# Optimization experiments

Measured on AMD Instinct MI355X. Metric: run time of the kernel, lower is better.

Reference implementation:

```python
import jax, jax.numpy as jnp
import numpy as np
from jax import lax

DIM = 64
NUM_HEADS = 1
HEAD_DIM = DIM // NUM_HEADS
SR = 8  # reduction_ratio
SCALE = HEAD_DIM ** -0.5


def setup_inputs() -> dict:
    key = jax.random.key(0)
    ks = jax.random.split(key, 12)
    s = 0.02
    return {
        "x": jax.random.normal(ks[0], (8, 16384, DIM), dtype=jnp.float32),
        # conv sr: (out_ch, in_ch, kH, kW) torch OIHW layout
        "sr_w": jax.random.normal(ks[1], (DIM, DIM, SR, SR), dtype=jnp.float32) * s,
        "sr_b": jnp.zeros((DIM,), jnp.float32),
        "ln_g": jnp.ones((DIM,), jnp.float32),
        "ln_b": jnp.zeros((DIM,), jnp.float32),
        # torch Linear weights: (out_features, in_features)
        "q_w": jax.random.normal(ks[2], (DIM, DIM), dtype=jnp.float32) * s,
        "q_b": jnp.zeros((DIM,), jnp.float32),
        "kv_w": jax.random.normal(ks[3], (2 * DIM, DIM), dtype=jnp.float32) * s,
        "kv_b": jnp.zeros((2 * DIM,), jnp.float32),
        "proj_w": jax.random.normal(ks[4], (DIM, DIM), dtype=jnp.float32) * s,
        "proj_b": jnp.zeros((DIM,), jnp.float32),
    }


def _layernorm(x, g, b, eps=1e-5):
    mu = jnp.mean(x, axis=-1, keepdims=True)
    var = jnp.var(x, axis=-1, keepdims=True)
    return (x - mu) * lax.rsqrt(var + eps) * g + b


def reference(x, sr_w, sr_b, ln_g, ln_b, q_w, q_b, kv_w, kv_b, proj_w, proj_b):
    B, N, C = x.shape
    H = W = int(N ** 0.5)
    # q: (B, heads, N, head_dim)
    q = (x @ q_w.T + q_b).reshape(B, N, NUM_HEADS, HEAD_DIM).transpose(0, 2, 1, 3)
    # spatial reduction of KV via strided conv + LayerNorm
    x_ = x.transpose(0, 2, 1).reshape(B, C, H, W)
    x_ = lax.conv_general_dilated(
        x_, sr_w, window_strides=(SR, SR), padding="VALID",
        dimension_numbers=("NCHW", "OIHW", "NCHW"))
    x_ = x_ + sr_b[None, :, None, None]
    x_ = x_.reshape(B, C, -1).transpose(0, 2, 1)  # (B, Nr, C)
    x_ = _layernorm(x_, ln_g, ln_b)
    Nr = x_.shape[1]
    kv = (x_ @ kv_w.T + kv_b).reshape(B, Nr, 2, NUM_HEADS, HEAD_DIM)
    kv = kv.transpose(2, 0, 3, 1, 4)  # (2, B, heads, Nr, hd)
    k, v = kv[0], kv[1]
    attn = jnp.einsum("bhnd,bhmd->bhnm", q, k) * SCALE
    attn = jax.nn.softmax(attn, axis=-1)
    out = jnp.einsum("bhnm,bhmd->bhnd", attn, v)
    out = out.transpose(0, 2, 1, 3).reshape(B, N, C)
    return out @ proj_w.T + proj_b
```

## Files before the change

kernel.cpp:

```cpp
#include <hip/hip_runtime.h>
#include <hip/hip_bf16.h>


typedef __attribute__((ext_vector_type(8))) short bf16x8;
typedef __attribute__((ext_vector_type(4))) float f32x4;

__device__ __forceinline__ unsigned short f2bf(float f) {
    union { __hip_bfloat16 h; unsigned short u; } cv;
    cv.h = __hip_bfloat16(f);
    return cv.u;
}
union U8 { uint4 u; bf16x8 v; };
__device__ __forceinline__ bf16x8 pack8(float e0,float e1,float e2,float e3,
                                        float e4,float e5,float e6,float e7){
    U8 r;
    r.u.x = (unsigned)f2bf(e0) | ((unsigned)f2bf(e1)<<16);
    r.u.y = (unsigned)f2bf(e2) | ((unsigned)f2bf(e3)<<16);
    r.u.z = (unsigned)f2bf(e4) | ((unsigned)f2bf(e5)<<16);
    r.u.w = (unsigned)f2bf(e6) | ((unsigned)f2bf(e7)<<16);
    return r.v;
}
__device__ __forceinline__ bf16x8 ldg8(const unsigned short* p){
    U8 r; r.u = *(const uint4*)p; return r.v;
}

__global__ __launch_bounds__(256) void prep_kernel(
    const float* __restrict__ sr_w,
    const float* __restrict__ q_w, const float* __restrict__ q_b,
    const float* __restrict__ proj_w,
    unsigned short* __restrict__ wbp,
    unsigned short* __restrict__ qwb, unsigned short* __restrict__ pwp,
    float* __restrict__ qb_s)
{
    int tid = blockIdx.x * 256 + threadIdx.x;
    {
        int i = tid & 7, n = (tid>>3)&15, g = (tid>>7)&3, ks = (tid>>9)&31,
            kc = (tid>>14)&3, w = tid>>16;
        int co = 16*w + n;
        int k  = kc*1024 + ks*32 + 8*g + i;
        int kh = k >> 9, kw = (k>>6)&7, cin = k & 63;
        wbp[tid] = f2bf(sr_w[co*4096 + cin*64 + kh*8 + kw]);
    }
    if (tid < 4096)   qwb[tid] = f2bf(q_w[tid] * 0.125f);
    if (tid < 4096) {
        int i = tid & 7, g = (tid>>3)&3, s3 = (tid>>5)&1, co = tid>>6;
        int ch = 32*s3 + 16*(i>>2) + 4*g + (i&3);
        pwp[tid] = f2bf(proj_w[co*64 + ch]);
    }
    if (tid < 64) qb_s[tid] = q_b[tid] * 0.125f;
}

__global__ __launch_bounds__(512) void convln_kernel(
    const float* __restrict__ x, const unsigned short* __restrict__ wbp,
    const float* __restrict__ sr_b,
    const float* __restrict__ ln_g, const float* __restrict__ ln_b,
    const float* __restrict__ kv_w, const float* __restrict__ kv_b,
    unsigned short* __restrict__ kbuf, unsigned short* __restrict__ vp)
{
    __shared__ uint4 xsm4[4096];
    char* xsm = (char*)xsm4;
    float* red = (float*)xsm;
    float* ysp = (float*)(xsm + 49152);

    int bid = blockIdx.x;
    int b = bid >> 4, oh = bid & 15;
    int t = threadIdx.x;
    int w = t >> 6, lane = t & 63, g = lane >> 4, n = lane & 15;

    f32x4 acc[4] = {{0,0,0,0},{0,0,0,0},{0,0,0,0},{0,0,0,0}};
    int khl = w >> 1;
    int kwh = w & 1;

    #pragma unroll
    for (int p = 0; p < 2; ++p) {
        const float* slab = x + (size_t)(b*128 + oh*8 + 4*p) * 128 * 64;
        #pragma unroll
        for (int c2 = 0; c2 < 8; ++c2) {
            int eo = (c2*512 + t) * 8;
            float4 v0 = *(const float4*)(slab + eo);
            float4 v1 = *(const float4*)(slab + eo + 4);
            int byte = eo * 2;
            int dst = byte ^ (((byte >> 10) & 7) << 4);
            U8 tmp; tmp.v = pack8(v0.x,v0.y,v0.z,v0.w,v1.x,v1.y,v1.z,v1.w);
            *(uint4*)(xsm + dst) = tmp.u;
        }
        __syncthreads();

        int khp = 4*p + khl;
        int kc  = khp >> 1;
        int swz = (n & 7) << 4;
        #pragma unroll
        for (int j = 0; j < 8; ++j) {
            int ks  = (khp & 1)*16 + kwh*8 + j;
            int kw  = kwh*4 + (j >> 1);
            int cb  = ((j & 1) << 5) + 8*g;
            int byte = khl*16384 + (n*8 + kw)*128 + cb*2;
            U8 Bx; Bx.u = *(const uint4*)(xsm + (byte ^ swz));
            #pragma unroll
            for (int tc = 0; tc < 4; ++tc) {
                bf16x8 A = ldg8(wbp + ((((tc*4 + kc)*32 + ks)*4 + g)*16 + n)*8);
                acc[tc] = __builtin_amdgcn_mfma_f32_16x16x32_bf16(A, Bx.v, acc[tc], 0, 0, 0);
            }
        }
        __syncthreads();
    }

    #pragma unroll
    for (int tc = 0; tc < 4; ++tc) {
        int byte = w*4096 + n*256 + (16*tc + 4*g)*4;
        *(f32x4*)(xsm + (byte ^ ((n & 7) << 4))) = acc[tc];
    }
    __syncthreads();

    int c = lane;
    #pragma unroll
    for (int pp = 0; pp < 2; ++pp) {
        int pos = w + 8*pp;
        int swzp = (pos & 7) << 4;
        float val = sr_b[c];
        #pragma unroll
        for (int w8 = 0; w8 < 8; ++w8)
            val += *(const float*)(xsm + ((w8*4096 + pos*256 + 4*c) ^ swzp));
        float s = val, s2 = val*val;
        #pragma unroll
        for (int o = 32; o >= 1; o >>= 1) {
            s  += __shfl_xor(s,  o, 64);
            s2 += __shfl_xor(s2, o, 64);
        }
        float mean = s * (1.f/64.f);
        float var  = s2 * (1.f/64.f) - mean*mean;
        float y = (val - mean) * rsqrtf(var + 1e-5f) * ln_g[c] + ln_b[c];
        ysp[pos*64 + c] = y;
        int m = oh*16 + pos;
        #pragma unroll
        for (int h = 0; h < 2; ++h) {
            int oc = c + h*64;
            float a2 = kv_b[oc];
            const float* wr = kv_w + oc*64;
            #pragma unroll
            for (int jj = 0; jj < 64; jj += 4) {
                float4 w4 = *(const float4*)(wr + jj);
                a2 += ysp[pos*64+jj]*w4.x + ysp[pos*64+jj+1]*w4.y
                    + ysp[pos*64+jj+2]*w4.z + ysp[pos*64+jj+3]*w4.w;
            }
            if (h == 0) {
                kbuf[(b*256 + m)*64 + c] = f2bf(a2);
            } else {
                int ks2 = m >> 5, hi = (m >> 4) & 1, g2 = (m >> 2) & 3, r = m & 3;
                vp[(size_t)b*16384 + ((ks2*4 + g2)*64 + c)*8 + r + 4*hi] = f2bf(a2);
            }
        }
    }
}

__global__ __launch_bounds__(512) void attn_kernel(
    const float* __restrict__ x,
    const unsigned short* __restrict__ qwb, const float* __restrict__ qb_s,
    const unsigned short* __restrict__ kbuf, const unsigned short* __restrict__ vp,
    const unsigned short* __restrict__ pwp, const float* __restrict__ proj_b,
    float* __restrict__ out)
{
    __shared__ char Ks[32768];
    int bid = blockIdx.x;
    int b = bid >> 7, rt = bid & 127;
    int t = threadIdx.x;
    {
        const char* kb = (const char*)(kbuf + (size_t)b*16384);
        #pragma unroll
        for (int c = 0; c < 4; ++c) {
            int off = (c*512 + t) * 16;
            int dst = off ^ (((off >> 7) & 7) << 4);
            *(uint4*)(Ks + dst) = *(const uint4*)(kb + off);
        }
    }
    __syncthreads();

    int w = t >> 6, lane = t & 63, g = lane >> 4, n = lane & 15;
    int qrow = rt*128 + w*16 + n;
    const float* xr = x + ((size_t)b*16384 + qrow) * 64;
    const char* vpb = (const char*)(vp + (size_t)b*16384);

    f32x4 qacc[4];
    #pragma unroll
    for (int tau = 0; tau < 4; ++tau)
        qacc[tau] = *(const f32x4*)(qb_s + 16*tau + 4*g);
    bf16x8 xq[2];
    #pragma unroll
    for (int s = 0; s < 2; ++s) {
        float4 v0 = *(const float4*)(xr + 32*s + 8*g);
        float4 v1 = *(const float4*)(xr + 32*s + 8*g + 4);
        xq[s] = pack8(v0.x,v0.y,v0.z,v0.w,v1.x,v1.y,v1.z,v1.w);
    }
    #pragma unroll
    for (int tau = 0; tau < 4; ++tau)
        #pragma unroll
        for (int s = 0; s < 2; ++s) {
            bf16x8 A = ldg8(qwb + (16*tau + n)*64 + 32*s + 8*g);
            qacc[tau] = __builtin_amdgcn_mfma_f32_16x16x32_bf16(A, xq[s], qacc[tau], 0,0,0);
        }
    bf16x8 qkB[2];
    #pragma unroll
    for (int s2 = 0; s2 < 2; ++s2)
        qkB[s2] = pack8(qacc[2*s2][0],  qacc[2*s2][1],  qacc[2*s2][2],  qacc[2*s2][3],
                        qacc[2*s2+1][0],qacc[2*s2+1][1],qacc[2*s2+1][2],qacc[2*s2+1][3]);

    float S[16][4];
    #pragma unroll
    for (int tt = 0; tt < 16; ++tt) {
        f32x4 sa = {0.f, 0.f, 0.f, 0.f};
        int m = 16*tt + n;
        int base = m * 128;
        int swz = (m & 7) << 4;
        #pragma unroll
        for (int s2 = 0; s2 < 2; ++s2) {
            int c1 = (32*s2 + 4*g) * 2;
            uint2 d0 = *(const uint2*)(Ks + ((base + c1)      ^ swz));
            uint2 d1 = *(const uint2*)(Ks + ((base + c1 + 32) ^ swz));
            U8 A; A.u = make_uint4(d0.x, d0.y, d1.x, d1.y);
            sa = __builtin_amdgcn_mfma_f32_16x16x32_bf16(A.v, qkB[s2], sa, 0,0,0);
        }
        S[tt][0]=sa[0]; S[tt][1]=sa[1]; S[tt][2]=sa[2]; S[tt][3]=sa[3];
    }

    float rm[16];
    #pragma unroll
    for (int tt = 0; tt < 16; ++tt)
        rm[tt] = fmaxf(fmaxf(S[tt][0],S[tt][1]), fmaxf(S[tt][2],S[tt][3]));
    float m8[8];
    #pragma unroll
    for (int j = 0; j < 8; ++j) m8[j] = fmaxf(rm[2*j], rm[2*j+1]);
    float mx = fmaxf(fmaxf(fmaxf(m8[0],m8[1]),fmaxf(m8[2],m8[3])),
                     fmaxf(fmaxf(m8[4],m8[5]),fmaxf(m8[6],m8[7])));
    mx = fmaxf(mx, __shfl_xor(mx, 16, 64));
    mx = fmaxf(mx, __shfl_xor(mx, 32, 64));
    #pragma unroll
    for (int tt = 0; tt < 16; ++tt)
        #pragma unroll
        for (int r = 0; r < 4; ++r)
            S[tt][r] = __expf(S[tt][r] - mx);
    float rs[16];
    #pragma unroll
    for (int tt = 0; tt < 16; ++tt) rs[tt] = (S[tt][0]+S[tt][1]) + (S[tt][2]+S[tt][3]);
    float s8[8];
    #pragma unroll
    for (int j = 0; j < 8; ++j) s8[j] = rs[2*j] + rs[2*j+1];
    float ssum = ((s8[0]+s8[1])+(s8[2]+s8[3])) + ((s8[4]+s8[5])+(s8[6]+s8[7]));
    ssum += __shfl_xor(ssum, 16, 64);
    ssum += __shfl_xor(ssum, 32, 64);
    float inv = 1.f / ssum;

    f32x4 oacc[4] = {{0,0,0,0},{0,0,0,0},{0,0,0,0},{0,0,0,0}};
    #pragma unroll
    for (int ks = 0; ks < 8; ++ks) {
        bf16x8 Bp = pack8(S[2*ks][0],  S[2*ks][1],  S[2*ks][2],  S[2*ks][3],
                          S[2*ks+1][0],S[2*ks+1][1],S[2*ks+1][2],S[2*ks+1][3]);
        #pragma unroll
        for (int tc = 0; tc < 4; ++tc) {
            U8 A; A.u = *(const uint4*)(vpb + ((ks*4 + g)*64 + 16*tc + n) * 16);
            oacc[tc] = __builtin_amdgcn_mfma_f32_16x16x32_bf16(A.v, Bp, oacc[tc], 0,0,0);
        }
    }

    bf16x8 Bo[2];
    #pragma unroll
    for (int s3 = 0; s3 < 2; ++s3)
        Bo[s3] = pack8(oacc[2*s3][0]*inv,   oacc[2*s3][1]*inv,
                       oacc[2*s3][2]*inv,   oacc[2*s3][3]*inv,
                       oacc[2*s3+1][0]*inv, oacc[2*s3+1][1]*inv,
                       oacc[2*s3+1][2]*inv, oacc[2*s3+1][3]*inv);
    f32x4 pacc[4];
    #pragma unroll
    for (int tf = 0; tf < 4; ++tf)
        pacc[tf] = *(const f32x4*)(proj_b + 16*tf + 4*g);
    #pragma unroll
    for (int tf = 0; tf < 4; ++tf)
        #pragma unroll
        for (int s3 = 0; s3 < 2; ++s3) {
            bf16x8 Aw = ldg8(pwp + (((16*tf + n)*2 + s3)*4 + g)*8);
            pacc[tf] = __builtin_amdgcn_mfma_f32_16x16x32_bf16(Aw, Bo[s3], pacc[tf], 0,0,0);
        }
    float* orow = out + ((size_t)b*16384 + qrow) * 64;
    #pragma unroll
    for (int tf = 0; tf < 4; ++tf)
        *(float4*)(orow + 16*tf + 4*g) = *(float4*)&pacc[tf];
}

extern "C" void kernel_launch(void* const* d_in, const int* in_sizes, int n_in,
                              void* d_out, int out_size, void* d_ws, size_t ws_size,
                              hipStream_t stream)
{
    const float* x      = (const float*)d_in[0];
    const float* sr_w   = (const float*)d_in[1];
    const float* sr_b   = (const float*)d_in[2];
    const float* ln_g   = (const float*)d_in[3];
    const float* ln_b   = (const float*)d_in[4];
    const float* q_w    = (const float*)d_in[5];
    const float* q_b    = (const float*)d_in[6];
    const float* kv_w   = (const float*)d_in[7];
    const float* kv_b   = (const float*)d_in[8];
    const float* proj_w = (const float*)d_in[9];
    const float* proj_b = (const float*)d_in[10];
    float* out = (float*)d_out;

    char* wsb = (char*)d_ws;
    unsigned short* wbp  = (unsigned short*)(wsb);
    unsigned short* kbuf = (unsigned short*)(wsb + 524288);
    unsigned short* vp   = (unsigned short*)(wsb + 786432);
    unsigned short* qwb  = (unsigned short*)(wsb + 1048576);
    unsigned short* pwp  = (unsigned short*)(wsb + 1056768);
    float*          qb_s = (float*)(wsb + 1064960);

    hipLaunchKernelGGL(prep_kernel, dim3(1024), dim3(256), 0, stream,
                       sr_w, q_w, q_b, proj_w, wbp, qwb, pwp, qb_s);
    hipLaunchKernelGGL(convln_kernel, dim3(128), dim3(512), 0, stream,
                       x, wbp, sr_b, ln_g, ln_b, kv_w, kv_b, kbuf, vp);
    hipLaunchKernelGGL(attn_kernel, dim3(1024), dim3(512), 0, stream,
                       x, qwb, qb_s, kbuf, vp, pwp, proj_b, out);
}
```

Measured before the change: 175.2 us.

## Split strided conv across four blocks per output row and coalesce weight prep

The conv+LayerNorm kernel now uses 512 blocks, each handling a quarter of an output row (4 output positions), instead of 128 blocks covering a full row. Each wave now owns one kernel row kh, and the weight layout is reordered to match. The prep kernel stages one output channel's weights in shared memory so it can read them coalesced and write packed 8-element bf16 vectors. The aim is better occupancy across the GPU's CUs and cheaper weight repacking. In exchange, many MFMA lanes are wasted since only 4 of 16 columns are useful, and each block re-reads the full weight tensor from global memory.

```diff
diff --git a/kernel.cpp b/kernel.cpp
--- a/kernel.cpp
+++ b/kernel.cpp
@@ -32,20 +32,34 @@
     unsigned short* __restrict__ qwb, unsigned short* __restrict__ pwp,
     float* __restrict__ qb_s)
 {
-    int tid = blockIdx.x * 256 + threadIdx.x;
-    {
-        int i = tid & 7, n = (tid>>3)&15, g = (tid>>7)&3, ks = (tid>>9)&31,
-            kc = (tid>>14)&3, w = tid>>16;
-        int co = 16*w + n;
-        int k  = kc*1024 + ks*32 + 8*g + i;
-        int kh = k >> 9, kw = (k>>6)&7, cin = k & 63;
-        wbp[tid] = f2bf(sr_w[co*4096 + cin*64 + kh*8 + kw]);
-    }
-    if (tid < 4096)   qwb[tid] = f2bf(q_w[tid] * 0.125f);
+    __shared__ float wsm[4096];
+    int co = blockIdx.x;
+    int t  = threadIdx.x;
+    #pragma unroll
+    for (int u = 0; u < 4; ++u) {
+        int e = (u*256 + t)*4;
+        *(float4*)&wsm[e] = *(const float4*)(sr_w + (size_t)co*4096 + e);
+    }
+    __syncthreads();
+    int tc = co >> 4, n = co & 15;
+    #pragma unroll
+    for (int u = 0; u < 2; ++u) {
+        int gidx = t*2 + u;
+        int g = gidx & 3, j = (gidx>>2) & 15, kh = gidx >> 6;
+        int kw = j >> 1, cinb = (j&1)*32 + 8*g;
+        float e[8];
+        #pragma unroll
+        for (int i = 0; i < 8; ++i)
+            e[i] = wsm[(cinb + i)*64 + kh*8 + kw];
+        U8 tmp; tmp.v = pack8(e[0],e[1],e[2],e[3],e[4],e[5],e[6],e[7]);
+        *(uint4*)(wbp + (size_t)((((kh*16 + j)*4 + tc)*4 + g)*16 + n)*8) = tmp.u;
+    }
+    int tid = co*256 + t;
+    if (tid < 4096) qwb[tid] = f2bf(q_w[tid] * 0.125f);
     if (tid < 4096) {
-        int i = tid & 7, g = (tid>>3)&3, s3 = (tid>>5)&1, co = tid>>6;
+        int i = tid & 7, g = (tid>>3)&3, s3 = (tid>>5)&1, co2 = tid>>6;
         int ch = 32*s3 + 16*(i>>2) + 4*g + (i&3);
-        pwp[tid] = f2bf(proj_w[co*64 + ch]);
+        pwp[tid] = f2bf(proj_w[co2*64 + ch]);
     }
     if (tid < 64) qb_s[tid] = q_b[tid] * 0.125f;
 }
@@ -57,70 +71,53 @@
     const float* __restrict__ kv_w, const float* __restrict__ kv_b,
     unsigned short* __restrict__ kbuf, unsigned short* __restrict__ vp)
 {
-    __shared__ uint4 xsm4[4096];
-    char* xsm = (char*)xsm4;
-    float* red = (float*)xsm;
-    float* ysp = (float*)(xsm + 49152);
-
+    __shared__ char xsm[32768];
     int bid = blockIdx.x;
-    int b = bid >> 4, oh = bid & 15;
+    int b = bid >> 6, oh = (bid >> 2) & 15, oq = bid & 3;
     int t = threadIdx.x;
     int w = t >> 6, lane = t & 63, g = lane >> 4, n = lane & 15;
 
+    #pragma unroll
+    for (int c2 = 0; c2 < 4; ++c2) {
+        int eo = (c2*512 + t) * 8;
+        int r = eo >> 11, inrow = eo & 2047;
+        const float* src = x + ((size_t)((b*128 + oh*8 + r)*128 + oq*32))*64 + inrow;
+        float4 v0 = *(const float4*)(src);
+        float4 v1 = *(const float4*)(src + 4);
+        U8 tmp; tmp.v = pack8(v0.x,v0.y,v0.z,v0.w,v1.x,v1.y,v1.z,v1.w);
+        *(uint4*)(xsm + eo*2) = tmp.u;
+    }
+    __syncthreads();
+
+    int pos = n & 3;
     f32x4 acc[4] = {{0,0,0,0},{0,0,0,0},{0,0,0,0},{0,0,0,0}};
-    int khl = w >> 1;
-    int kwh = w & 1;
-
-    #pragma unroll
-    for (int p = 0; p < 2; ++p) {
-        const float* slab = x + (size_t)(b*128 + oh*8 + 4*p) * 128 * 64;
-        #pragma unroll
-        for (int c2 = 0; c2 < 8; ++c2) {
-            int eo = (c2*512 + t) * 8;
-            float4 v0 = *(const float4*)(slab + eo);
-            float4 v1 = *(const float4*)(slab + eo + 4);
-            int byte = eo * 2;
-            int dst = byte ^ (((byte >> 10) & 7) << 4);
-            U8 tmp; tmp.v = pack8(v0.x,v0.y,v0.z,v0.w,v1.x,v1.y,v1.z,v1.w);
-            *(uint4*)(xsm + dst) = tmp.u;
-        }
-        __syncthreads();
-
-        int khp = 4*p + khl;
-        int kc  = khp >> 1;
-        int swz = (n & 7) << 4;
-        #pragma unroll
-        for (int j = 0; j < 8; ++j) {
-            int ks  = (khp & 1)*16 + kwh*8 + j;
-            int kw  = kwh*4 + (j >> 1);
-            int cb  = ((j & 1) << 5) + 8*g;
-            int byte = khl*16384 + (n*8 + kw)*128 + cb*2;
-            U8 Bx; Bx.u = *(const uint4*)(xsm + (byte ^ swz));
-            #pragma unroll
-            for (int tc = 0; tc < 4; ++tc) {
-                bf16x8 A = ldg8(wbp + ((((tc*4 + kc)*32 + ks)*4 + g)*16 + n)*8);
-                acc[tc] = __builtin_amdgcn_mfma_f32_16x16x32_bf16(A, Bx.v, acc[tc], 0, 0, 0);
-            }
-        }
-        __syncthreads();
-    }
-
-    #pragma unroll
-    for (int tc = 0; tc < 4; ++tc) {
-        int byte = w*4096 + n*256 + (16*tc + 4*g)*4;
-        *(f32x4*)(xsm + (byte ^ ((n & 7) << 4))) = acc[tc];
-    }
-    __syncthreads();
-
-    int c = lane;
-    #pragma unroll
-    for (int pp = 0; pp < 2; ++pp) {
-        int pos = w + 8*pp;
-        int swzp = (pos & 7) << 4;
+    #pragma unroll
+    for (int j = 0; j < 16; ++j) {
+        int byte = ((w*32 + pos*8 + (j>>1))*64 + (j&1)*32 + 8*g) * 2;
+        U8 Bx; Bx.u = *(const uint4*)(xsm + byte);
+        #pragma unroll
+        for (int tc = 0; tc < 4; ++tc) {
+            bf16x8 A = ldg8(wbp + (size_t)((((w*16 + j)*4 + tc)*4 + g)*16 + n)*8);
+            acc[tc] = __builtin_amdgcn_mfma_f32_16x16x32_bf16(A, Bx.v, acc[tc], 0, 0, 0);
+        }
+    }
+    __syncthreads();
+
+    float* red = (float*)xsm;
+    float* ysp = (float*)(xsm + 8192);
+    if (n < 4) {
+        #pragma unroll
+        for (int tc = 0; tc < 4; ++tc)
+            *(f32x4*)(red + (w*4 + n)*64 + 16*tc + 4*g) = acc[tc];
+    }
+    __syncthreads();
+
+    if (w < 4) {
+        int p = w, c = lane;
         float val = sr_b[c];
         #pragma unroll
         for (int w8 = 0; w8 < 8; ++w8)
-            val += *(const float*)(xsm + ((w8*4096 + pos*256 + 4*c) ^ swzp));
+            val += red[(w8*4 + p)*64 + c];
         float s = val, s2 = val*val;
         #pragma unroll
         for (int o = 32; o >= 1; o >>= 1) {
@@ -130,8 +127,13 @@
         float mean = s * (1.f/64.f);
         float var  = s2 * (1.f/64.f) - mean*mean;
         float y = (val - mean) * rsqrtf(var + 1e-5f) * ln_g[c] + ln_b[c];
-        ysp[pos*64 + c] = y;
-        int m = oh*16 + pos;
+        ysp[p*64 + c] = y;
+    }
+    __syncthreads();
+    if (w < 4) {
+        int p = w, c = lane;
+        int m = oh*16 + oq*4 + p;
+        const float* yr = ysp + p*64;
         #pragma unroll
         for (int h = 0; h < 2; ++h) {
             int oc = c + h*64;
@@ -140,8 +142,7 @@
             #pragma unroll
             for (int jj = 0; jj < 64; jj += 4) {
                 float4 w4 = *(const float4*)(wr + jj);
-                a2 += ysp[pos*64+jj]*w4.x + ysp[pos*64+jj+1]*w4.y
-                    + ysp[pos*64+jj+2]*w4.z + ysp[pos*64+jj+3]*w4.w;
+                a2 += yr[jj]*w4.x + yr[jj+1]*w4.y + yr[jj+2]*w4.z + yr[jj+3]*w4.w;
             }
             if (h == 0) {
                 kbuf[(b*256 + m)*64 + c] = f2bf(a2);
@@ -310,9 +311,9 @@
     unsigned short* pwp  = (unsigned short*)(wsb + 1056768);
     float*          qb_s = (float*)(wsb + 1064960);
 
-    hipLaunchKernelGGL(prep_kernel, dim3(1024), dim3(256), 0, stream,
+    hipLaunchKernelGGL(prep_kernel, dim3(64), dim3(256), 0, stream,
                        sr_w, q_w, q_b, proj_w, wbp, qwb, pwp, qb_s);
-    hipLaunchKernelGGL(convln_kernel, dim3(128), dim3(512), 0, stream,
+    hipLaunchKernelGGL(convln_kernel, dim3(512), dim3(512), 0, stream,
                        x, wbp, sr_b, ln_g, ln_b, kv_w, kv_b, kbuf, vp);
     hipLaunchKernelGGL(attn_kernel, dim3(1024), dim3(512), 0, stream,
                        x, qwb, qb_s, kbuf, vp, pwp, proj_b, out);
```

After: 157.1 us. 10.3% less time.
